# Kernel optimization log

Hardware: AMD Instinct MI355X
Metric: run time of the kernel (lower is better)

## Reference

```python
import jax, jax.numpy as jnp
import numpy as np

B, S, DQK, DV, H = 4, 2048, 128, 128, 8


def setup_inputs() -> dict:
    key = jax.random.key(0)
    ks = jax.random.split(key, 9)
    s = 0.02
    return {
        "query": jax.random.normal(ks[0], (B, S, DQK), jnp.float32),
        "key": jax.random.normal(ks[1], (B, S, DQK), jnp.float32),
        "value": jax.random.normal(ks[2], (B, S, DV), jnp.float32),
        "WQ": jax.random.normal(ks[3], (DQK, H * DQK), jnp.float32) * s,
        "bQ": jax.random.normal(ks[4], (H * DQK,), jnp.float32) * s,
        "WK": jax.random.normal(ks[5], (DQK, H * DQK), jnp.float32) * s,
        "bK": jax.random.normal(ks[6], (H * DQK,), jnp.float32) * s,
        "WV": jax.random.normal(ks[7], (DV, H * DV), jnp.float32) * s,
        "bV": jax.random.normal(ks[8], (H * DV,), jnp.float32) * s,
    }


def reference(query, key, value, WQ, bQ, WK, bK, WV, bV):
    b, qn, dqk = query.shape
    kn = key.shape[1]
    dv = value.shape[2]
    h = H
    # projections -> [b, n, h, d]
    Q = (query @ WQ + bQ).reshape(b, qn, h, dqk)
    K = (key @ WK + bK).reshape(b, kn, h, dqk)
    V = (value @ WV + bV).reshape(b, kn, h, dv)
    # abs(QK^T)/sqrt(dk) score -- non-standard, prevents flash kernels
    scores = jnp.abs(jnp.einsum("bqhd,bkhd->bhqk", Q, K)) / jnp.sqrt(
        jnp.asarray(dqk, query.dtype)
    )
    w = jax.nn.softmax(scores, axis=-1)  # [b,h,q,k]
    # (complex cast +0j in the original is numerically a no-op on real V)
    out = jnp.einsum("bhqk,bkhd->bqhd", w, V).reshape(b, qn, h * dv)
    return out
```

## Files before the change

### kernel.cpp

```cpp
#include <hip/hip_runtime.h>
#include <hip/hip_bf16.h>

#define B_ 4
#define S_ 2048
#define D_ 128
#define H_ 8

typedef __attribute__((ext_vector_type(8))) short bf16x8;
typedef __attribute__((ext_vector_type(4))) float f32x4;

__device__ __forceinline__ short f2bf(float f) {
  union { float f; unsigned u; } v; v.f = f;
  unsigned u = v.u;
  unsigned r = (u + 0x7FFFu + ((u >> 16) & 1u)) >> 16;
  return (short)r;
}

__device__ __forceinline__ short4 pack4(f32x4 p) {
  union { __hip_bfloat162 h2[2]; short4 s4; } u;
  u.h2[0] = __float22bfloat162_rn(make_float2(p[0], p[1]));
  u.h2[1] = __float22bfloat162_rn(make_float2(p[2], p[3]));
  return u.s4;
}

__device__ __forceinline__ void dma16(const short* g, short* l) {
  __builtin_amdgcn_global_load_lds(
      (const __attribute__((address_space(1))) unsigned int*)g,
      (__attribute__((address_space(3))) unsigned int*)l, 16, 0, 0);
}

__global__ __launch_bounds__(256) void prep(
    const float* __restrict__ WQ, const float* __restrict__ WK, const float* __restrict__ WV,
    short* __restrict__ TQ, short* __restrict__ TK, short* __restrict__ TV) {
  __shared__ float tile[64][65];
  int bw = blockIdx.x >> 5;
  int tl = blockIdx.x & 31;
  int n0 = (tl & 15) * 64, k0 = (tl >> 4) * 64;
  const float* W = (bw == 0) ? WQ : (bw == 1) ? WK : WV;
  short* Wt = (bw == 0) ? TQ : (bw == 1) ? TK : TV;
#pragma unroll
  for (int i = 0; i < 16; ++i) {
    int cix = threadIdx.x + 256 * i;
    int rr = cix >> 6, cc = cix & 63;
    tile[rr][cc] = W[(k0 + rr) * 1024 + n0 + cc];
  }
  __syncthreads();
#pragma unroll
  for (int i = 0; i < 16; ++i) {
    int cix = threadIdx.x + 256 * i;
    int rr = cix >> 6, cc = cix & 63;
    Wt[(n0 + rr) * 128 + k0 + cc] = f2bf(tile[cc][rr]);
  }
}

template <int MODE>
__device__ __forceinline__ void proj_tile(const float* __restrict__ X,
                                          const short* __restrict__ Wt,
                                          const float* __restrict__ bias,
                                          short* __restrict__ out,
                                          int mtile, int ntile,
                                          short* sA, short* sB) {
  int tid = threadIdx.x;
  int lane = tid & 63, w = tid >> 6;
  int l15 = lane & 15, l4 = lane >> 4;
  int m0 = mtile * 128, n0 = ntile * 128;

#pragma unroll
  for (int j = 0; j < 8; ++j) {
    int f = w * 8 + j;
    const short* src = Wt + (n0 + (f >> 2) * 16 + l15) * 128 + (f & 3) * 32 + l4 * 8;
    dma16(src, sB + f * 512);
  }
#pragma unroll
  for (int j = 0; j < 8; ++j) {
    int f = w * 8 + j;
    const float* src = X + (size_t)(m0 + (f >> 2) * 16 + l15) * 128 + (f & 3) * 32 + l4 * 8;
    float4 v0 = *(const float4*)src;
    float4 v1 = *(const float4*)(src + 4);
    union { struct { short4 lo, hi; } s; bf16x8 v; } u;
    u.s.lo = pack4((f32x4){v0.x, v0.y, v0.z, v0.w});
    u.s.hi = pack4((f32x4){v1.x, v1.y, v1.z, v1.w});
    *(bf16x8*)(sA + f * 512 + lane * 8) = u.v;
  }
  __syncthreads();

  int wr = w >> 1, wc = w & 1;
  f32x4 acc[4][4];
#pragma unroll
  for (int mi = 0; mi < 4; ++mi)
#pragma unroll
    for (int ni = 0; ni < 4; ++ni) acc[mi][ni] = (f32x4){0.f, 0.f, 0.f, 0.f};

#pragma unroll
  for (int mi = 0; mi < 4; ++mi) {
    bf16x8 a[4];
#pragma unroll
    for (int st = 0; st < 4; ++st)
      a[st] = *(const bf16x8*)(sA + ((wr * 4 + mi) * 4 + st) * 512 + lane * 8);
#pragma unroll
    for (int ni = 0; ni < 4; ++ni) {
#pragma unroll
      for (int st = 0; st < 4; ++st) {
        bf16x8 b = *(const bf16x8*)(sB + ((wc * 4 + ni) * 4 + st) * 512 + lane * 8);
        if (MODE <= 1)
          acc[mi][ni] = __builtin_amdgcn_mfma_f32_16x16x32_bf16(b, a[st], acc[mi][ni], 0, 0, 0);
        else
          acc[mi][ni] = __builtin_amdgcn_mfma_f32_16x16x32_bf16(a[st], b, acc[mi][ni], 0, 0, 0);
      }
    }
  }

  if (MODE == 0) {
#pragma unroll
    for (int mi = 0; mi < 4; ++mi) {
      int sg = m0 + wr * 64 + mi * 16 + l15;
      int bb = sg >> 11, s = sg & 2047;
      short* orow = out + ((size_t)(bb * H_ + ntile) * S_ + s) * D_;
#pragma unroll
      for (int ni = 0; ni < 4; ++ni) {
        int d0 = wc * 64 + ni * 16 + l4 * 4;
        float4 bv = *(const float4*)(bias + n0 + d0);
        f32x4 t = acc[mi][ni];
        t[0] += bv.x; t[1] += bv.y; t[2] += bv.z; t[3] += bv.w;
        *(short4*)(orow + d0) = pack4(t);
      }
    }
  } else if (MODE == 1) {
#pragma unroll
    for (int mi = 0; mi < 4; ++mi) {
      int key = m0 + wr * 64 + mi * 16 + l15;
      int bb = key >> 11, k = key & 2047;
      size_t base = (size_t)(bb * H_ + ntile) * (S_ * D_) + (size_t)(k >> 6) * 8192
                  + ((k >> 4) & 3) * 4 * 512 + (k & 15) * 8;
#pragma unroll
      for (int ni = 0; ni < 4; ++ni) {
        int d0 = wc * 64 + ni * 16 + l4 * 4;
        float4 bv = *(const float4*)(bias + n0 + d0);
        f32x4 t = acc[mi][ni];
        t[0] += bv.x; t[1] += bv.y; t[2] += bv.z; t[3] += bv.w;
        size_t off = base + (size_t)(d0 >> 5) * 512 + ((d0 >> 3) & 3) * 128 + (d0 & 7);
        *(short4*)(out + off) = pack4(t);
      }
    }
  } else {
#pragma unroll
    for (int ni = 0; ni < 4; ++ni) {
      int d = wc * 64 + ni * 16 + l15;
      float bvs = bias[n0 + d];
#pragma unroll
      for (int mi = 0; mi < 4; ++mi) {
        int sg0 = m0 + wr * 64 + mi * 16 + l4 * 4;
        int bb = sg0 >> 11, s0 = sg0 & 2047;
        f32x4 t = acc[mi][ni];
        t[0] += bvs; t[1] += bvs; t[2] += bvs; t[3] += bvs;
        size_t off = (size_t)(bb * H_ + ntile) * (S_ * D_)
                   + (size_t)(s0 >> 6) * 8192
                   + (size_t)((d >> 4) * 2 + ((s0 >> 5) & 1)) * 512
                   + ((s0 >> 3) & 3) * 128 + (d & 15) * 8
                   + (s0 & 7);
        *(short4*)(out + off) = pack4(t);
      }
    }
  }
}

__global__ __launch_bounds__(256, 3) void proj3(
    const float* __restrict__ xq, const float* __restrict__ xk, const float* __restrict__ xv,
    const short* __restrict__ wtq, const short* __restrict__ wtk, const short* __restrict__ wtv,
    const float* __restrict__ bQ, const float* __restrict__ bK, const float* __restrict__ bV,
    short* __restrict__ Qp, short* __restrict__ Kf, short* __restrict__ Vf) {
  __shared__ short sA[16384], sB[16384];
  int work = (blockIdx.x & 7) * 192 + (blockIdx.x >> 3);
  int which = work >> 9;
  int t = work & 511;
  int mtile = t >> 3, ntile = t & 7;
  if (which == 0)      proj_tile<0>(xq, wtq, bQ, Qp, mtile, ntile, sA, sB);
  else if (which == 1) proj_tile<1>(xk, wtk, bK, Kf, mtile, ntile, sA, sB);
  else                 proj_tile<2>(xv, wtv, bV, Vf, mtile, ntile, sA, sB);
}

#define PSTR 72

#define QK_CLUSTER()                                                           \
  _Pragma("unroll") for (int mt = 0; mt < 4; ++mt) {                           \
    s0[mt] = (f32x4){0.f, 0.f, 0.f, 0.f};                                      \
    s1[mt] = (f32x4){0.f, 0.f, 0.f, 0.f};                                      \
    _Pragma("unroll") for (int st = 0; st < 4; ++st) {                         \
      s0[mt] = __builtin_amdgcn_mfma_f32_16x16x32_bf16(kf[mt * 4 + st], aq[0][st], s0[mt], 0, 0, 0); \
      s1[mt] = __builtin_amdgcn_mfma_f32_16x16x32_bf16(kf[mt * 4 + st], aq[1][st], s1[mt], 0, 0, 0); \
    }                                                                          \
  }

#define SM_CLUSTER()                                                           \
  _Pragma("unroll") for (int mt = 0; mt < 4; ++mt) {                           \
    _Pragma("unroll") for (int r = 0; r < 4; ++r) {                            \
      float p = __builtin_amdgcn_exp2f(fabsf(s0[mt][r]) * SC2);                \
      ls0 += p;                                                                \
      s0[mt][r] = p;                                                           \
    }                                                                          \
    *(short4*)(pw + l15 * PSTR + mt * 16 + l4 * 4) = pack4(s0[mt]);            \
  }                                                                            \
  ap0[0] = *(const bf16x8*)(pw + l15 * PSTR + l4 * 8);                         \
  ap0[1] = *(const bf16x8*)(pw + l15 * PSTR + 32 + l4 * 8);                    \
  _Pragma("unroll") for (int mt = 0; mt < 4; ++mt) {                           \
    _Pragma("unroll") for (int r = 0; r < 4; ++r) {                            \
      float p = __builtin_amdgcn_exp2f(fabsf(s1[mt][r]) * SC2);                \
      ls1 += p;                                                                \
      s1[mt][r] = p;                                                           \
    }                                                                          \
    *(short4*)(pw + l15 * PSTR + mt * 16 + l4 * 4) = pack4(s1[mt]);            \
  }                                                                            \
  ap1[0] = *(const bf16x8*)(pw + l15 * PSTR + l4 * 8);                         \
  ap1[1] = *(const bf16x8*)(pw + l15 * PSTR + 32 + l4 * 8);

#define PV_CLUSTER()                                                           \
  _Pragma("unroll") for (int t8 = 0; t8 < 8; ++t8) {                           \
    _Pragma("unroll") for (int kst = 0; kst < 2; ++kst) {                      \
      o0[t8] = __builtin_amdgcn_mfma_f32_16x16x32_bf16(ap0[kst], bv[t8 * 2 + kst], o0[t8], 0, 0, 0); \
      o1[t8] = __builtin_amdgcn_mfma_f32_16x16x32_bf16(ap1[kst], bv[t8 * 2 + kst], o1[t8], 0, 0, 0); \
    }                                                                          \
  }

__global__ __launch_bounds__(256, 2) void attn(const short* __restrict__ Qp,
                                               const short* __restrict__ Kf,
                                               const short* __restrict__ Vf,
                                               float* __restrict__ out) {
  __shared__ short sP[4 * 16 * PSTR];

  int tid = threadIdx.x;
  int lane = tid & 63, w = tid >> 6;
  int swz = (blockIdx.x & 7) * 64 + (blockIdx.x >> 3);
  int qt = swz & 15;
  int bh = swz >> 4;
  int q0 = qt * 128;
  int l15 = lane & 15, l4 = lane >> 4;

  const short* Qbase = Qp + (size_t)bh * S_ * D_;
  const short* kfb = Kf + (size_t)bh * S_ * D_ + lane * 8;
  const short* vfb = Vf + (size_t)bh * S_ * D_ + lane * 8;

  bf16x8 aq[2][4];
#pragma unroll
  for (int g = 0; g < 2; ++g)
#pragma unroll
    for (int st = 0; st < 4; ++st)
      aq[g][st] = *(const bf16x8*)(Qbase + (q0 + w * 32 + g * 16 + l15) * D_ + l4 * 8 + 32 * st);

  f32x4 o0[8], o1[8];
#pragma unroll
  for (int t = 0; t < 8; ++t) {
    o0[t] = (f32x4){0.f, 0.f, 0.f, 0.f};
    o1[t] = (f32x4){0.f, 0.f, 0.f, 0.f};
  }
  float ls0 = 0.f, ls1 = 0.f;

  const float SC2 = 0.127530637f;
  short* pw = sP + w * 16 * PSTR;

  for (int t = 0; t < S_ / 64; ++t) {
    bf16x8 kf[16];
#pragma unroll
    for (int f = 0; f < 16; ++f)
      kf[f] = *(const bf16x8*)(kfb + t * 8192 + f * 512);
    bf16x8 bv[16];
#pragma unroll
    for (int f = 0; f < 16; ++f)
      bv[f] = *(const bf16x8*)(vfb + t * 8192 + f * 512);
    __builtin_amdgcn_sched_barrier(0);

    f32x4 s0[4], s1[4];
    __builtin_amdgcn_s_setprio(1);
    QK_CLUSTER();
    __builtin_amdgcn_s_setprio(0);
    bf16x8 ap0[2], ap1[2];
    SM_CLUSTER();
    __builtin_amdgcn_s_setprio(1);
    PV_CLUSTER();
    __builtin_amdgcn_s_setprio(0);
  }

  ls0 += __shfl_xor(ls0, 16);
  ls0 += __shfl_xor(ls0, 32);
  ls1 += __shfl_xor(ls1, 16);
  ls1 += __shfl_xor(ls1, 32);
  float inv0[4], inv1[4];
#pragma unroll
  for (int r = 0; r < 4; ++r) {
    inv0[r] = 1.f / __shfl(ls0, l4 * 4 + r);
    inv1[r] = 1.f / __shfl(ls1, l4 * 4 + r);
  }

  int bb = bh >> 3, h = bh & 7;
#pragma unroll
  for (int t = 0; t < 8; ++t) {
#pragma unroll
    for (int r = 0; r < 4; ++r) {
      int qA = q0 + w * 32 + l4 * 4 + r;
      int qB = qA + 16;
      out[((size_t)(bb * S_ + qA)) * (H_ * D_) + h * D_ + t * 16 + l15] = o0[t][r] * inv0[r];
      out[((size_t)(bb * S_ + qB)) * (H_ * D_) + h * D_ + t * 16 + l15] = o1[t][r] * inv1[r];
    }
  }
}

extern "C" void kernel_launch(void* const* d_in, const int* in_sizes, int n_in,
                              void* d_out, int out_size, void* d_ws, size_t ws_size,
                              hipStream_t stream) {
  (void)in_sizes; (void)n_in; (void)out_size; (void)ws_size;
  const float* q  = (const float*)d_in[0];
  const float* k  = (const float*)d_in[1];
  const float* v  = (const float*)d_in[2];
  const float* WQ = (const float*)d_in[3];
  const float* bQ = (const float*)d_in[4];
  const float* WK = (const float*)d_in[5];
  const float* bK = (const float*)d_in[6];
  const float* WV = (const float*)d_in[7];
  const float* bV = (const float*)d_in[8];

  const int NW = D_ * H_ * D_;
  const int NP = B_ * H_ * S_ * D_;

  short* ws  = (short*)d_ws;
  short* wtq = ws;
  short* wtk = wtq + NW;
  short* wtv = wtk + NW;
  short* Qp  = wtv + NW;
  short* Kf  = Qp + NP;
  short* Vf  = Kf + NP;

  prep<<<96, 256, 0, stream>>>(WQ, WK, WV, wtq, wtk, wtv);

  proj3<<<1536, 256, 0, stream>>>(q, k, v, wtq, wtk, wtv, bQ, bK, bV, Qp, Kf, Vf);

  attn<<<512, 256, 0, stream>>>(Qp, Kf, Vf, (float*)d_out);
}
```

Baseline: 194.8 us.

## Split attention KV loop into half-steps with K register double-buffering

```diff
diff --git a/kernel.cpp b/kernel.cpp
--- a/kernel.cpp
+++ b/kernel.cpp
@@ -181,44 +181,52 @@
 
 #define PSTR 72
 
-#define QK_CLUSTER()                                                           \
-  _Pragma("unroll") for (int mt = 0; mt < 4; ++mt) {                           \
-    s0[mt] = (f32x4){0.f, 0.f, 0.f, 0.f};                                      \
-    s1[mt] = (f32x4){0.f, 0.f, 0.f, 0.f};                                      \
-    _Pragma("unroll") for (int st = 0; st < 4; ++st) {                         \
-      s0[mt] = __builtin_amdgcn_mfma_f32_16x16x32_bf16(kf[mt * 4 + st], aq[0][st], s0[mt], 0, 0, 0); \
-      s1[mt] = __builtin_amdgcn_mfma_f32_16x16x32_bf16(kf[mt * 4 + st], aq[1][st], s1[mt], 0, 0, 0); \
-    }                                                                          \
-  }
-
-#define SM_CLUSTER()                                                           \
-  _Pragma("unroll") for (int mt = 0; mt < 4; ++mt) {                           \
-    _Pragma("unroll") for (int r = 0; r < 4; ++r) {                            \
-      float p = __builtin_amdgcn_exp2f(fabsf(s0[mt][r]) * SC2);                \
-      ls0 += p;                                                                \
-      s0[mt][r] = p;                                                           \
-    }                                                                          \
-    *(short4*)(pw + l15 * PSTR + mt * 16 + l4 * 4) = pack4(s0[mt]);            \
-  }                                                                            \
-  ap0[0] = *(const bf16x8*)(pw + l15 * PSTR + l4 * 8);                         \
-  ap0[1] = *(const bf16x8*)(pw + l15 * PSTR + 32 + l4 * 8);                    \
-  _Pragma("unroll") for (int mt = 0; mt < 4; ++mt) {                           \
-    _Pragma("unroll") for (int r = 0; r < 4; ++r) {                            \
-      float p = __builtin_amdgcn_exp2f(fabsf(s1[mt][r]) * SC2);                \
-      ls1 += p;                                                                \
-      s1[mt][r] = p;                                                           \
-    }                                                                          \
-    *(short4*)(pw + l15 * PSTR + mt * 16 + l4 * 4) = pack4(s1[mt]);            \
-  }                                                                            \
-  ap1[0] = *(const bf16x8*)(pw + l15 * PSTR + l4 * 8);                         \
-  ap1[1] = *(const bf16x8*)(pw + l15 * PSTR + 32 + l4 * 8);
-
-#define PV_CLUSTER()                                                           \
-  _Pragma("unroll") for (int t8 = 0; t8 < 8; ++t8) {                           \
-    _Pragma("unroll") for (int kst = 0; kst < 2; ++kst) {                      \
-      o0[t8] = __builtin_amdgcn_mfma_f32_16x16x32_bf16(ap0[kst], bv[t8 * 2 + kst], o0[t8], 0, 0, 0); \
-      o1[t8] = __builtin_amdgcn_mfma_f32_16x16x32_bf16(ap1[kst], bv[t8 * 2 + kst], o1[t8], 0, 0, 0); \
-    }                                                                          \
+#define HSTEP(KC, KN, H, DOISS)                                                \
+  {                                                                            \
+    if (DOISS) {                                                               \
+      _Pragma("unroll") for (int j = 0; j < 8; ++j)                            \
+        KN[j] = *(const bf16x8*)(kfb + ((H) + 1) * 4096 + j * 512);            \
+    }                                                                          \
+    bf16x8 bv[8];                                                              \
+    _Pragma("unroll") for (int j = 0; j < 8; ++j)                              \
+      bv[j] = *(const bf16x8*)(vfb + ((H) >> 1) * 8192 + (j * 2 + ((H) & 1)) * 512); \
+    __builtin_amdgcn_sched_barrier(0);                                         \
+    f32x4 s0[2], s1[2];                                                        \
+    __builtin_amdgcn_s_setprio(1);                                             \
+    _Pragma("unroll") for (int m = 0; m < 2; ++m) {                            \
+      s0[m] = (f32x4){0.f, 0.f, 0.f, 0.f};                                     \
+      s1[m] = (f32x4){0.f, 0.f, 0.f, 0.f};                                     \
+      _Pragma("unroll") for (int st = 0; st < 4; ++st) {                       \
+        s0[m] = __builtin_amdgcn_mfma_f32_16x16x32_bf16(KC[m * 4 + st], aq[0][st], s0[m], 0, 0, 0); \
+        s1[m] = __builtin_amdgcn_mfma_f32_16x16x32_bf16(KC[m * 4 + st], aq[1][st], s1[m], 0, 0, 0); \
+      }                                                                        \
+    }                                                                          \
+    __builtin_amdgcn_s_setprio(0);                                             \
+    bf16x8 ap0, ap1;                                                           \
+    _Pragma("unroll") for (int m = 0; m < 2; ++m) {                            \
+      _Pragma("unroll") for (int r = 0; r < 4; ++r) {                          \
+        float p = __builtin_amdgcn_exp2f(fabsf(s0[m][r]) * SC2);               \
+        ls0 += p;                                                              \
+        s0[m][r] = p;                                                          \
+      }                                                                        \
+      *(short4*)(pw + l15 * PSTR + m * 16 + l4 * 4) = pack4(s0[m]);            \
+    }                                                                          \
+    ap0 = *(const bf16x8*)(pw + l15 * PSTR + l4 * 8);                          \
+    _Pragma("unroll") for (int m = 0; m < 2; ++m) {                            \
+      _Pragma("unroll") for (int r = 0; r < 4; ++r) {                          \
+        float p = __builtin_amdgcn_exp2f(fabsf(s1[m][r]) * SC2);               \
+        ls1 += p;                                                              \
+        s1[m][r] = p;                                                          \
+      }                                                                        \
+      *(short4*)(pw + l15 * PSTR + m * 16 + l4 * 4) = pack4(s1[m]);            \
+    }                                                                          \
+    ap1 = *(const bf16x8*)(pw + l15 * PSTR + l4 * 8);                          \
+    __builtin_amdgcn_s_setprio(1);                                             \
+    _Pragma("unroll") for (int t8 = 0; t8 < 8; ++t8) {                         \
+      o0[t8] = __builtin_amdgcn_mfma_f32_16x16x32_bf16(ap0, bv[t8], o0[t8], 0, 0, 0); \
+      o1[t8] = __builtin_amdgcn_mfma_f32_16x16x32_bf16(ap1, bv[t8], o1[t8], 0, 0, 0); \
+    }                                                                          \
+    __builtin_amdgcn_s_setprio(0);                                             \
   }
 
 __global__ __launch_bounds__(256, 2) void attn(const short* __restrict__ Qp,
@@ -229,9 +237,10 @@
 
   int tid = threadIdx.x;
   int lane = tid & 63, w = tid >> 6;
-  int swz = (blockIdx.x & 7) * 64 + (blockIdx.x >> 3);
-  int qt = swz & 15;
-  int bh = swz >> 4;
+  int xcd = blockIdx.x & 7;
+  int idx = blockIdx.x >> 3;
+  int bh  = xcd * 4 + (idx & 3);
+  int qt  = idx >> 2;
   int q0 = qt * 128;
   int l15 = lane & 15, l4 = lane >> 4;
 
@@ -257,26 +266,14 @@
   const float SC2 = 0.127530637f;
   short* pw = sP + w * 16 * PSTR;
 
-  for (int t = 0; t < S_ / 64; ++t) {
-    bf16x8 kf[16];
-#pragma unroll
-    for (int f = 0; f < 16; ++f)
-      kf[f] = *(const bf16x8*)(kfb + t * 8192 + f * 512);
-    bf16x8 bv[16];
-#pragma unroll
-    for (int f = 0; f < 16; ++f)
-      bv[f] = *(const bf16x8*)(vfb + t * 8192 + f * 512);
-    __builtin_amdgcn_sched_barrier(0);
-
-    f32x4 s0[4], s1[4];
-    __builtin_amdgcn_s_setprio(1);
-    QK_CLUSTER();
-    __builtin_amdgcn_s_setprio(0);
-    bf16x8 ap0[2], ap1[2];
-    SM_CLUSTER();
-    __builtin_amdgcn_s_setprio(1);
-    PV_CLUSTER();
-    __builtin_amdgcn_s_setprio(0);
+  bf16x8 kfA[8], kfB[8];
+#pragma unroll
+  for (int j = 0; j < 8; ++j)
+    kfA[j] = *(const bf16x8*)(kfb + j * 512);
+
+  for (int t = 0; t < 32; ++t) {
+    HSTEP(kfA, kfB, 2 * t, true);
+    HSTEP(kfB, kfA, 2 * t + 1, (t < 31));
   }
 
   ls0 += __shfl_xor(ls0, 16);
```

Measured after the change: 186.2 us. 4.4% less time.
